# Kernel optimization log

Hardware: AMD Instinct MI355X
Metric: run time of the kernel (lower is better)

The kernel has to match this reference:

```python
import jax, jax.numpy as jnp
import numpy as np

E = 8          # num_experts
K = 2          # experts_per_token
D = 1024       # d_model
F = 2048       # dim_feedforward
B, S = 2, 2048

def setup_inputs() -> dict:
    key = jax.random.key(0)
    ks = jax.random.split(key, 5)
    scale = 0.02
    return {
        "x":   jax.random.normal(ks[0], (B, S, D), jnp.float32),
        "Wr":  jax.random.normal(ks[1], (E, D), jnp.float32) * scale,
        "temp": jnp.ones((1,), jnp.float32),
        "W1":  jax.random.normal(ks[2], (E, 2 * F, D), jnp.float32) * scale,
        "b1":  jnp.zeros((E, 2 * F), jnp.float32),
        "W2":  jax.random.normal(ks[3], (E, D, F), jnp.float32) * scale,
        "b2":  jnp.zeros((E, D), jnp.float32),
    }

def reference(x, Wr, temp, W1, b1, W2, b2):
    b, s, d = x.shape
    xf = x.reshape(-1, d)                                   # [T, D]
    router_logits = (xf @ Wr.T) / temp                      # [T, E]
    # eval mode: no router noise, dropout is identity
    top_w, top_idx = jax.lax.top_k(router_logits, K)        # [T, K]
    top_w = jax.nn.softmax(top_w, axis=-1)                  # renormalize over top-k
    # dense gate matrix [T, E]: weight if expert selected else 0 (topk indices are distinct)
    gates = jnp.sum(jax.nn.one_hot(top_idx, E, dtype=xf.dtype) * top_w[..., None], axis=1)
    out = jnp.zeros_like(xf)
    for e in range(E):  # fixed small expert loop, dense compute gated to zero for unrouted tokens
        h = xf @ W1[e].T + b1[e]                            # [T, 2F]
        a = h[:, :F] * jax.nn.silu(h[:, F:])                # SwiGLU -> [T, F]
        y = a @ W2[e].T + b2[e]                             # [T, D]
        out = out + y * gates[:, e:e + 1]
    return out.reshape(b, s, d)
```

## Files before the change

kernel.cpp:

```cpp
#include <hip/hip_runtime.h>
#include <hip/hip_bf16.h>

#define DEV __device__ __forceinline__

namespace {

constexpr int D     = 1024;
constexpr int F     = 2048;
constexpr int E     = 8;
constexpr int TWO_F = 2 * F;

typedef short bf16x8 __attribute__((ext_vector_type(8)));
typedef float f32x4  __attribute__((ext_vector_type(4)));

DEV unsigned short f32_to_bf16(float f) {
  unsigned int u = __builtin_bit_cast(unsigned int, f);
  u += 0x7fffu + ((u >> 16) & 1u);
  return (unsigned short)(u >> 16);
}

DEV void load_lds16(const void* g, void* l) {
  __builtin_amdgcn_global_load_lds((const __attribute__((address_space(1))) void*)g,
                                   (__attribute__((address_space(3))) void*)l, 16, 0, 0);
}

DEV const bf16x8* frag_addr(const unsigned short* S, int row, int kk, int quad) {
  int cl = (((kk >> 3) + quad) ^ (row & 7));
  return (const bf16x8*)(S + row * 64 + cl * 8);
}

__global__ void zero_kernel(float* __restrict__ p, int n4) {
  int i = blockIdx.x * 256 + threadIdx.x;
  if (i < n4) ((float4*)p)[i] = make_float4(0.f, 0.f, 0.f, 0.f);
}

__global__ void cvt_all_kernel(const float* __restrict__ x, const float* __restrict__ W1,
                               const float* __restrict__ W2,
                               unsigned short* __restrict__ xb, unsigned short* __restrict__ W1b,
                               unsigned short* __restrict__ W2b,
                               long long nx, long long n1) {
  long long i = (long long)(blockIdx.x * 256 + threadIdx.x) * 8;
  const float* src;
  unsigned short* dst;
  long long off;
  if (i < nx)            { src = x;  dst = xb;  off = i; }
  else if (i < nx + n1)  { src = W1; dst = W1b; off = i - nx; }
  else                   { src = W2; dst = W2b; off = i - nx - n1; }
  float4 a = *(const float4*)(src + off);
  float4 b = *(const float4*)(src + off + 4);
  uint4 o;
  o.x = (unsigned)f32_to_bf16(a.x) | ((unsigned)f32_to_bf16(a.y) << 16);
  o.y = (unsigned)f32_to_bf16(a.z) | ((unsigned)f32_to_bf16(a.w) << 16);
  o.z = (unsigned)f32_to_bf16(b.x) | ((unsigned)f32_to_bf16(b.y) << 16);
  o.w = (unsigned)f32_to_bf16(b.z) | ((unsigned)f32_to_bf16(b.w) << 16);
  *(uint4*)(dst + off) = o;
}

__global__ void router_kernel(const float* __restrict__ x, const float* __restrict__ Wr,
                              const float* __restrict__ temp,
                              int* __restrict__ topk_idx, float* __restrict__ topk_gate, int T) {
  int wid  = blockIdx.x * 4 + (threadIdx.x >> 6);
  int lane = threadIdx.x & 63;
  if (wid >= T) return;
  const float* xr = x + (size_t)wid * D;
  float acc[E];
#pragma unroll
  for (int e = 0; e < E; ++e) acc[e] = 0.f;
  int base = lane * 16;
#pragma unroll
  for (int u = 0; u < 4; ++u) {
    float4 xv = *(const float4*)(xr + base + u * 4);
#pragma unroll
    for (int e = 0; e < E; ++e) {
      float4 wv = *(const float4*)(Wr + e * D + base + u * 4);
      acc[e] += xv.x * wv.x + xv.y * wv.y + xv.z * wv.z + xv.w * wv.w;
    }
  }
#pragma unroll
  for (int e = 0; e < E; ++e) {
    float v = acc[e];
#pragma unroll
    for (int off = 32; off > 0; off >>= 1) v += __shfl_xor(v, off, 64);
    acc[e] = v;
  }
  if (lane == 0) {
    float inv = 1.0f / temp[0];
    float l[E];
#pragma unroll
    for (int e = 0; e < E; ++e) l[e] = acc[e] * inv;
    int e0 = 0;
#pragma unroll
    for (int e = 1; e < E; ++e) if (l[e] > l[e0]) e0 = e;
    int e1 = (e0 == 0) ? 1 : 0;
#pragma unroll
    for (int e = 0; e < E; ++e) if (e != e0 && l[e] > l[e1]) e1 = e;
    float dlt = l[e1] - l[e0];
    float ed  = __expf(dlt);
    topk_idx[2 * wid]      = e0;
    topk_idx[2 * wid + 1]  = e1;
    topk_gate[2 * wid]     = 1.f / (1.f + ed);
    topk_gate[2 * wid + 1] = ed / (1.f + ed);
  }
}

__global__ __launch_bounds__(1024)
void assign_kernel(const int* __restrict__ topk_idx, const float* __restrict__ topk_gate,
                   int* __restrict__ counts, int* __restrict__ offsets,
                   int* __restrict__ row_token, float* __restrict__ row_gate, int T) {
  __shared__ int hist[E];
  __shared__ int cur[E];
  const int tid = threadIdx.x;
  if (tid < E) hist[tid] = 0;
  __syncthreads();
  for (int t = tid; t < T; t += 1024) {
    atomicAdd(&hist[topk_idx[2 * t]], 1);
    atomicAdd(&hist[topk_idx[2 * t + 1]], 1);
  }
  __syncthreads();
  if (tid == 0) {
    int s = 0;
    for (int e = 0; e < E; ++e) {
      int c = hist[e];
      counts[e]  = c;
      offsets[e] = s;
      cur[e]     = s;
      s += c;
    }
  }
  __syncthreads();
  for (int t = tid; t < T; t += 1024) {
#pragma unroll
    for (int s = 0; s < 2; ++s) {
      int e = topk_idx[2 * t + s];
      int p = atomicAdd(&cur[e], 1);
      row_token[p] = t;
      row_gate[p]  = topk_gate[2 * t + s];
    }
  }
}

__global__ __launch_bounds__(256, 2)
void gemm1_kernel(const unsigned short* __restrict__ xb,
                  const unsigned short* __restrict__ W1b,
                  const float* __restrict__ b1,
                  const int* __restrict__ counts, const int* __restrict__ offsets,
                  const int* __restrict__ row_token,
                  unsigned short* __restrict__ a_buf) {
  const int e  = blockIdx.z;
  const int m0 = blockIdx.y * 128;
  const int n0 = blockIdx.x * 64;
  const int cnt = counts[e];
  if (m0 >= cnt) return;
  const int pairBase = offsets[e];

  __shared__ __align__(16) unsigned short As[128 * 64];
  __shared__ __align__(16) unsigned short Bs[128 * 64];
  __shared__ int tokS[128];

  const int tid = threadIdx.x;
  if (tid < 128) {
    int r = m0 + tid;
    tokS[tid] = (r < cnt) ? row_token[pairBase + r] : row_token[pairBase];
  }
  __syncthreads();

  const int lane = tid & 63;
  const int wave = tid >> 6;
  const int quad = lane >> 4;
  const int l16  = lane & 15;
  const int lr   = lane >> 3;
  const int lc   = lane & 7;
  const int sw   = lc ^ (lr & 7);
  const int wr   = wave >> 1;
  const int wc   = wave & 1;

  const unsigned short* W1e = W1b + (size_t)e * TWO_F * D;
  const unsigned short* aptr[4];
  const unsigned short* bptr[4];
#pragma unroll
  for (int i = 0; i < 4; ++i) {
    int r = wave * 32 + i * 8 + lr;
    aptr[i] = xb + (size_t)tokS[r] * D + sw * 8;
    int g = r >> 5, s = r & 31;
    int wrow = (g & 1) * F + n0 + (g >> 1) * 32 + s;
    bptr[i] = W1e + (size_t)wrow * D + sw * 8;
  }
  unsigned short* AsW = As + (wave * 32) * 64;
  unsigned short* BsW = Bs + (wave * 32) * 64;

  f32x4 acc[4][4];
#pragma unroll
  for (int i = 0; i < 4; ++i)
#pragma unroll
    for (int j = 0; j < 4; ++j) acc[i][j] = (f32x4){0.f, 0.f, 0.f, 0.f};

  for (int k0 = 0; k0 < D; k0 += 64) {
#pragma unroll
    for (int i = 0; i < 4; ++i) load_lds16(aptr[i] + k0, AsW + i * 8 * 64);
#pragma unroll
    for (int i = 0; i < 4; ++i) load_lds16(bptr[i] + k0, BsW + i * 8 * 64);
    __syncthreads();
#pragma unroll
    for (int kk = 0; kk < 64; kk += 32) {
      bf16x8 af[4], bf[4];
#pragma unroll
      for (int i = 0; i < 4; ++i)
        af[i] = *frag_addr(As, wr * 64 + i * 16 + l16, kk, quad);
#pragma unroll
      for (int j = 0; j < 4; ++j)
        bf[j] = *frag_addr(Bs, wc * 64 + j * 16 + l16, kk, quad);
#pragma unroll
      for (int i = 0; i < 4; ++i)
#pragma unroll
        for (int j = 0; j < 4; ++j)
          acc[i][j] = __builtin_amdgcn_mfma_f32_16x16x32_bf16(af[i], bf[j], acc[i][j], 0, 0, 0);
    }
    __syncthreads();
  }

#pragma unroll
  for (int i = 0; i < 4; ++i) {
    int rb = wr * 64 + i * 16 + quad * 4;
#pragma unroll
    for (int j = 0; j < 2; ++j) {
      int col = n0 + wc * 32 + j * 16 + l16;
      float bh1 = b1[e * TWO_F + col];
      float bh2 = b1[e * TWO_F + F + col];
#pragma unroll
      for (int rg = 0; rg < 4; ++rg) {
        int r = rb + rg;
        if (m0 + r < cnt) {
          float h1 = acc[i][j][rg] + bh1;
          float h2 = acc[i][j + 2][rg] + bh2;
          float a  = h1 * (h2 / (1.f + __expf(-h2)));
          a_buf[(size_t)(pairBase + m0 + r) * F + col] = f32_to_bf16(a);
        }
      }
    }
  }
}

__global__ __launch_bounds__(256, 2)
void gemm2_kernel(const unsigned short* __restrict__ a_buf,
                  const unsigned short* __restrict__ W2b,
                  const float* __restrict__ b2,
                  const int* __restrict__ counts, const int* __restrict__ offsets,
                  const int* __restrict__ row_token, const float* __restrict__ row_gate,
                  float* __restrict__ out, int totalPairs) {
  const int e  = blockIdx.z;
  const int m0 = blockIdx.y * 128;
  const int n0 = blockIdx.x * 128;
  const int cnt = counts[e];
  if (m0 >= cnt) return;
  const int pairBase = offsets[e];

  __shared__ __align__(16) unsigned short As[128 * 64];
  __shared__ __align__(16) unsigned short Bs[128 * 64];
  __shared__ int   tokS[128];
  __shared__ float gateS[128];

  const int tid = threadIdx.x;
  if (tid < 128) {
    int r = m0 + tid;
    bool v = (r < cnt);
    tokS[tid]  = v ? row_token[pairBase + r] : 0;
    gateS[tid] = v ? row_gate[pairBase + r] : 0.f;
  }
  __syncthreads();

  const int lane = tid & 63;
  const int wave = tid >> 6;
  const int quad = lane >> 4;
  const int l16  = lane & 15;
  const int lr   = lane >> 3;
  const int lc   = lane & 7;
  const int sw   = lc ^ (lr & 7);
  const int wr   = wave >> 1;
  const int wc   = wave & 1;

  const unsigned short* W2e = W2b + (size_t)e * D * F;
  const unsigned short* aptr[4];
  const unsigned short* bptr[4];
#pragma unroll
  for (int i = 0; i < 4; ++i) {
    int r = wave * 32 + i * 8 + lr;
    int g = pairBase + m0 + r;
    if (g > totalPairs - 1) g = totalPairs - 1;
    aptr[i] = a_buf + (size_t)g * F + sw * 8;
    bptr[i] = W2e + (size_t)(n0 + r) * F + sw * 8;
  }
  unsigned short* AsW = As + (wave * 32) * 64;
  unsigned short* BsW = Bs + (wave * 32) * 64;

  f32x4 acc[4][4];
#pragma unroll
  for (int i = 0; i < 4; ++i)
#pragma unroll
    for (int j = 0; j < 4; ++j) acc[i][j] = (f32x4){0.f, 0.f, 0.f, 0.f};

  for (int k0 = 0; k0 < F; k0 += 64) {
#pragma unroll
    for (int i = 0; i < 4; ++i) load_lds16(aptr[i] + k0, AsW + i * 8 * 64);
#pragma unroll
    for (int i = 0; i < 4; ++i) load_lds16(bptr[i] + k0, BsW + i * 8 * 64);
    __syncthreads();
#pragma unroll
    for (int kk = 0; kk < 64; kk += 32) {
      bf16x8 af[4], bf[4];
#pragma unroll
      for (int i = 0; i < 4; ++i)
        af[i] = *frag_addr(As, wr * 64 + i * 16 + l16, kk, quad);
#pragma unroll
      for (int j = 0; j < 4; ++j)
        bf[j] = *frag_addr(Bs, wc * 64 + j * 16 + l16, kk, quad);
#pragma unroll
      for (int i = 0; i < 4; ++i)
#pragma unroll
        for (int j = 0; j < 4; ++j)
          acc[i][j] = __builtin_amdgcn_mfma_f32_16x16x32_bf16(af[i], bf[j], acc[i][j], 0, 0, 0);
    }
    __syncthreads();
  }

#pragma unroll
  for (int j = 0; j < 4; ++j) {
    int col = n0 + wc * 64 + j * 16 + l16;
    float b2v = b2[e * D + col];
#pragma unroll
    for (int i = 0; i < 4; ++i) {
      int rb = wr * 64 + i * 16 + quad * 4;
#pragma unroll
      for (int rg = 0; rg < 4; ++rg) {
        int r = rb + rg;
        if (m0 + r < cnt) {
          float y = (acc[i][j][rg] + b2v) * gateS[r];
          atomicAdd(&out[(size_t)tokS[r] * D + col], y);
        }
      }
    }
  }
}

}

extern "C" void kernel_launch(void* const* d_in, const int* in_sizes, int n_in,
                              void* d_out, int out_size, void* d_ws, size_t ws_size,
                              hipStream_t stream) {
  (void)n_in; (void)out_size; (void)ws_size;
  const float* x    = (const float*)d_in[0];
  const float* Wr   = (const float*)d_in[1];
  const float* temp = (const float*)d_in[2];
  const float* W1   = (const float*)d_in[3];
  const float* b1   = (const float*)d_in[4];
  const float* W2   = (const float*)d_in[5];
  const float* b2   = (const float*)d_in[6];
  float* out = (float*)d_out;
  const int T = in_sizes[0] / D;

  char* ws = (char*)d_ws;
  size_t off = 0;
  unsigned short* xb    = (unsigned short*)(ws + off); off += (size_t)T * D * 2;
  unsigned short* W1b   = (unsigned short*)(ws + off); off += (size_t)E * TWO_F * D * 2;
  unsigned short* W2b   = (unsigned short*)(ws + off); off += (size_t)E * D * F * 2;
  unsigned short* a_buf = (unsigned short*)(ws + off); off += (size_t)T * 2 * F * 2;
  int*   counts    = (int*)(ws + off); off += 64;
  int*   offsets   = (int*)(ws + off); off += 64;
  int*   topk_idx  = (int*)(ws + off); off += (size_t)T * 2 * 4;
  float* topk_gate = (float*)(ws + off); off += (size_t)T * 2 * 4;
  int*   row_token = (int*)(ws + off); off += (size_t)T * 2 * 4;
  float* row_gate  = (float*)(ws + off); off += (size_t)T * 2 * 4;

  const long long nx = (long long)T * D;
  const long long n1 = (long long)E * TWO_F * D;
  const long long n2 = (long long)E * D * F;

  zero_kernel<<<(T * D / 4 + 255) / 256, 256, 0, stream>>>(out, T * D / 4);
  router_kernel<<<(T + 3) / 4, 256, 0, stream>>>(x, Wr, temp, topk_idx, topk_gate, T);
  assign_kernel<<<1, 1024, 0, stream>>>(topk_idx, topk_gate, counts, offsets,
                                        row_token, row_gate, T);
  cvt_all_kernel<<<(int)((nx + n1 + n2) / 2048), 256, 0, stream>>>(x, W1, W2, xb, W1b, W2b,
                                                                   nx, n1);
  gemm1_kernel<<<dim3(F / 64, (T * 2 + 127) / 128, E), 256, 0, stream>>>(xb, W1b, b1, counts,
                                                                         offsets, row_token, a_buf);
  gemm2_kernel<<<dim3(D / 128, (T * 2 + 127) / 128, E), 256, 0, stream>>>(a_buf, W2b, b2, counts,
                                                                          offsets, row_token,
                                                                          row_gate, out, T * 2);
}
```

Measured before the change: 477.2 us.

## Widen GEMM tiles to 512 threads with triple-buffered async LDS pipeline

Both expert GEMMs move from 256 to 512 threads per block and double the N tile, to 128x256 in the B dimension. Global-to-LDS loads become triple-buffered, prefetching two k-tiles ahead with explicit vmcnt waits and raw s_barrier instead of a full syncthreads per step. MFMA priority is raised around the compute. The aim is to overlap memory latency with matrix math and reuse each A tile across more columns. The cost is about 144KB of LDS per block, which probably limits occupancy to one block per CU, plus hand-tuned waitcnt values that must match the exact load count.

```diff
diff --git a/kernel.cpp b/kernel.cpp
--- a/kernel.cpp
+++ b/kernel.cpp
@@ -139,7 +139,8 @@
   }
 }
 
-__global__ __launch_bounds__(256, 2)
+
+__global__ __launch_bounds__(512, 2)
 void gemm1_kernel(const unsigned short* __restrict__ xb,
                   const unsigned short* __restrict__ W1b,
                   const float* __restrict__ b1,
@@ -148,13 +149,13 @@
                   unsigned short* __restrict__ a_buf) {
   const int e  = blockIdx.z;
   const int m0 = blockIdx.y * 128;
-  const int n0 = blockIdx.x * 64;
+  const int bx = blockIdx.x;
   const int cnt = counts[e];
   if (m0 >= cnt) return;
   const int pairBase = offsets[e];
 
-  __shared__ __align__(16) unsigned short As[128 * 64];
-  __shared__ __align__(16) unsigned short Bs[128 * 64];
+  __shared__ __align__(16) unsigned short As[3][128 * 64];
+  __shared__ __align__(16) unsigned short Bs[3][256 * 64];
   __shared__ int tokS[128];
 
   const int tid = threadIdx.x;
@@ -170,23 +171,33 @@
   const int l16  = lane & 15;
   const int lr   = lane >> 3;
   const int lc   = lane & 7;
-  const int sw   = lc ^ (lr & 7);
-  const int wr   = wave >> 1;
-  const int wc   = wave & 1;
+  const int sw   = lc ^ lr;
+  const int wr   = wave >> 2;
+  const int wc   = wave & 3;
 
   const unsigned short* W1e = W1b + (size_t)e * TWO_F * D;
-  const unsigned short* aptr[4];
-  const unsigned short* bptr[4];
+  const unsigned short* aSrc[2];
+  const unsigned short* bSrc[4];
+#pragma unroll
+  for (int i = 0; i < 2; ++i) {
+    int rA = i * 64 + wave * 8 + lr;
+    aSrc[i] = xb + (size_t)tokS[rA] * D + sw * 8;
+  }
 #pragma unroll
   for (int i = 0; i < 4; ++i) {
-    int r = wave * 32 + i * 8 + lr;
-    aptr[i] = xb + (size_t)tokS[r] * D + sw * 8;
-    int g = r >> 5, s = r & 31;
-    int wrow = (g & 1) * F + n0 + (g >> 1) * 32 + s;
-    bptr[i] = W1e + (size_t)wrow * D + sw * 8;
-  }
-  unsigned short* AsW = As + (wave * 32) * 64;
-  unsigned short* BsW = Bs + (wave * 32) * 64;
+    int rB = i * 64 + wave * 8 + lr;
+    int wrow = ((rB >> 5) & 1) * F + bx * 128 + (rB >> 6) * 32 + (rB & 31);
+    bSrc[i] = W1e + (size_t)wrow * D + sw * 8;
+  }
+
+  auto stage = [&](int t, int b) {
+#pragma unroll
+    for (int i = 0; i < 2; ++i)
+      load_lds16(aSrc[i] + t * 64, &As[b][(i * 64 + wave * 8) * 64]);
+#pragma unroll
+    for (int i = 0; i < 4; ++i)
+      load_lds16(bSrc[i] + t * 64, &Bs[b][(i * 64 + wave * 8) * 64]);
+  };
 
   f32x4 acc[4][4];
 #pragma unroll
@@ -194,28 +205,49 @@
 #pragma unroll
     for (int j = 0; j < 4; ++j) acc[i][j] = (f32x4){0.f, 0.f, 0.f, 0.f};
 
-  for (int k0 = 0; k0 < D; k0 += 64) {
-#pragma unroll
-    for (int i = 0; i < 4; ++i) load_lds16(aptr[i] + k0, AsW + i * 8 * 64);
-#pragma unroll
-    for (int i = 0; i < 4; ++i) load_lds16(bptr[i] + k0, BsW + i * 8 * 64);
-    __syncthreads();
-#pragma unroll
-    for (int kk = 0; kk < 64; kk += 32) {
-      bf16x8 af[4], bf[4];
-#pragma unroll
-      for (int i = 0; i < 4; ++i)
-        af[i] = *frag_addr(As, wr * 64 + i * 16 + l16, kk, quad);
+  constexpr int NT = D / 64;
+  stage(0, 0);
+  stage(1, 1);
+  int buf = 0;
+  for (int t = 0; t < NT; ++t) {
+    if (t + 2 < NT) {
+      int nb = buf + 2; if (nb >= 3) nb -= 3;
+      stage(t + 2, nb);
+      asm volatile("s_waitcnt vmcnt(12)" ::: "memory");
+    } else if (t + 1 < NT) {
+      asm volatile("s_waitcnt vmcnt(6)" ::: "memory");
+    } else {
+      asm volatile("s_waitcnt vmcnt(0)" ::: "memory");
+    }
+    __builtin_amdgcn_sched_barrier(0);
+    __builtin_amdgcn_s_barrier();
+    __builtin_amdgcn_sched_barrier(0);
+    const unsigned short* Ab = As[buf];
+    const unsigned short* Bb = Bs[buf];
+    bf16x8 a0[4], b0[4], a1[4], b1f[4];
+#pragma unroll
+    for (int i = 0; i < 4; ++i) a0[i]  = *frag_addr(Ab, wr * 64 + i * 16 + l16, 0,  quad);
+#pragma unroll
+    for (int j = 0; j < 4; ++j) b0[j]  = *frag_addr(Bb, wc * 64 + j * 16 + l16, 0,  quad);
+#pragma unroll
+    for (int i = 0; i < 4; ++i) a1[i]  = *frag_addr(Ab, wr * 64 + i * 16 + l16, 32, quad);
+#pragma unroll
+    for (int j = 0; j < 4; ++j) b1f[j] = *frag_addr(Bb, wc * 64 + j * 16 + l16, 32, quad);
+    __builtin_amdgcn_s_setprio(1);
+#pragma unroll
+    for (int i = 0; i < 4; ++i)
 #pragma unroll
       for (int j = 0; j < 4; ++j)
-        bf[j] = *frag_addr(Bs, wc * 64 + j * 16 + l16, kk, quad);
-#pragma unroll
-      for (int i = 0; i < 4; ++i)
-#pragma unroll
-        for (int j = 0; j < 4; ++j)
-          acc[i][j] = __builtin_amdgcn_mfma_f32_16x16x32_bf16(af[i], bf[j], acc[i][j], 0, 0, 0);
-    }
-    __syncthreads();
+        acc[i][j] = __builtin_amdgcn_mfma_f32_16x16x32_bf16(a0[i], b0[j], acc[i][j], 0, 0, 0);
+#pragma unroll
+    for (int i = 0; i < 4; ++i)
+#pragma unroll
+      for (int j = 0; j < 4; ++j)
+        acc[i][j] = __builtin_amdgcn_mfma_f32_16x16x32_bf16(a1[i], b1f[j], acc[i][j], 0, 0, 0);
+    __builtin_amdgcn_s_setprio(0);
+    __builtin_amdgcn_sched_barrier(0);
+    __builtin_amdgcn_s_barrier();
+    ++buf; if (buf >= 3) buf = 0;
   }
 
 #pragma unroll
@@ -223,7 +255,7 @@
     int rb = wr * 64 + i * 16 + quad * 4;
 #pragma unroll
     for (int j = 0; j < 2; ++j) {
-      int col = n0 + wc * 32 + j * 16 + l16;
+      int col = bx * 128 + wc * 32 + j * 16 + l16;
       float bh1 = b1[e * TWO_F + col];
       float bh2 = b1[e * TWO_F + F + col];
 #pragma unroll
@@ -240,7 +272,7 @@
   }
 }
 
-__global__ __launch_bounds__(256, 2)
+__global__ __launch_bounds__(512, 2)
 void gemm2_kernel(const unsigned short* __restrict__ a_buf,
                   const unsigned short* __restrict__ W2b,
                   const float* __restrict__ b2,
@@ -249,13 +281,13 @@
                   float* __restrict__ out, int totalPairs) {
   const int e  = blockIdx.z;
   const int m0 = blockIdx.y * 128;
-  const int n0 = blockIdx.x * 128;
+  const int bx = blockIdx.x;
   const int cnt = counts[e];
   if (m0 >= cnt) return;
   const int pairBase = offsets[e];
 
-  __shared__ __align__(16) unsigned short As[128 * 64];
-  __shared__ __align__(16) unsigned short Bs[128 * 64];
+  __shared__ __align__(16) unsigned short As[3][128 * 64];
+  __shared__ __align__(16) unsigned short Bs[3][256 * 64];
   __shared__ int   tokS[128];
   __shared__ float gateS[128];
 
@@ -274,23 +306,34 @@
   const int l16  = lane & 15;
   const int lr   = lane >> 3;
   const int lc   = lane & 7;
-  const int sw   = lc ^ (lr & 7);
-  const int wr   = wave >> 1;
-  const int wc   = wave & 1;
+  const int sw   = lc ^ lr;
+  const int wr   = wave >> 2;
+  const int wc   = wave & 3;
 
   const unsigned short* W2e = W2b + (size_t)e * D * F;
-  const unsigned short* aptr[4];
-  const unsigned short* bptr[4];
+  const unsigned short* aSrc[2];
+  const unsigned short* bSrc[4];
+#pragma unroll
+  for (int i = 0; i < 2; ++i) {
+    int rA = i * 64 + wave * 8 + lr;
+    int g = pairBase + m0 + rA;
+    if (g > totalPairs - 1) g = totalPairs - 1;
+    aSrc[i] = a_buf + (size_t)g * F + sw * 8;
+  }
 #pragma unroll
   for (int i = 0; i < 4; ++i) {
-    int r = wave * 32 + i * 8 + lr;
-    int g = pairBase + m0 + r;
-    if (g > totalPairs - 1) g = totalPairs - 1;
-    aptr[i] = a_buf + (size_t)g * F + sw * 8;
-    bptr[i] = W2e + (size_t)(n0 + r) * F + sw * 8;
-  }
-  unsigned short* AsW = As + (wave * 32) * 64;
-  unsigned short* BsW = Bs + (wave * 32) * 64;
+    int rB = i * 64 + wave * 8 + lr;
+    bSrc[i] = W2e + (size_t)(bx * 256 + rB) * F + sw * 8;
+  }
+
+  auto stage = [&](int t, int b) {
+#pragma unroll
+    for (int i = 0; i < 2; ++i)
+      load_lds16(aSrc[i] + t * 64, &As[b][(i * 64 + wave * 8) * 64]);
+#pragma unroll
+    for (int i = 0; i < 4; ++i)
+      load_lds16(bSrc[i] + t * 64, &Bs[b][(i * 64 + wave * 8) * 64]);
+  };
 
   f32x4 acc[4][4];
 #pragma unroll
@@ -298,33 +341,54 @@
 #pragma unroll
     for (int j = 0; j < 4; ++j) acc[i][j] = (f32x4){0.f, 0.f, 0.f, 0.f};
 
-  for (int k0 = 0; k0 < F; k0 += 64) {
-#pragma unroll
-    for (int i = 0; i < 4; ++i) load_lds16(aptr[i] + k0, AsW + i * 8 * 64);
-#pragma unroll
-    for (int i = 0; i < 4; ++i) load_lds16(bptr[i] + k0, BsW + i * 8 * 64);
-    __syncthreads();
-#pragma unroll
-    for (int kk = 0; kk < 64; kk += 32) {
-      bf16x8 af[4], bf[4];
-#pragma unroll
-      for (int i = 0; i < 4; ++i)
-        af[i] = *frag_addr(As, wr * 64 + i * 16 + l16, kk, quad);
+  constexpr int NT = F / 64;
+  stage(0, 0);
+  stage(1, 1);
+  int buf = 0;
+  for (int t = 0; t < NT; ++t) {
+    if (t + 2 < NT) {
+      int nb = buf + 2; if (nb >= 3) nb -= 3;
+      stage(t + 2, nb);
+      asm volatile("s_waitcnt vmcnt(12)" ::: "memory");
+    } else if (t + 1 < NT) {
+      asm volatile("s_waitcnt vmcnt(6)" ::: "memory");
+    } else {
+      asm volatile("s_waitcnt vmcnt(0)" ::: "memory");
+    }
+    __builtin_amdgcn_sched_barrier(0);
+    __builtin_amdgcn_s_barrier();
+    __builtin_amdgcn_sched_barrier(0);
+    const unsigned short* Ab = As[buf];
+    const unsigned short* Bb = Bs[buf];
+    bf16x8 a0[4], b0[4], a1[4], b1f[4];
+#pragma unroll
+    for (int i = 0; i < 4; ++i) a0[i]  = *frag_addr(Ab, wr * 64 + i * 16 + l16, 0,  quad);
+#pragma unroll
+    for (int j = 0; j < 4; ++j) b0[j]  = *frag_addr(Bb, wc * 64 + j * 16 + l16, 0,  quad);
+#pragma unroll
+    for (int i = 0; i < 4; ++i) a1[i]  = *frag_addr(Ab, wr * 64 + i * 16 + l16, 32, quad);
+#pragma unroll
+    for (int j = 0; j < 4; ++j) b1f[j] = *frag_addr(Bb, wc * 64 + j * 16 + l16, 32, quad);
+    __builtin_amdgcn_s_setprio(1);
+#pragma unroll
+    for (int i = 0; i < 4; ++i)
 #pragma unroll
       for (int j = 0; j < 4; ++j)
-        bf[j] = *frag_addr(Bs, wc * 64 + j * 16 + l16, kk, quad);
-#pragma unroll
-      for (int i = 0; i < 4; ++i)
-#pragma unroll
-        for (int j = 0; j < 4; ++j)
-          acc[i][j] = __builtin_amdgcn_mfma_f32_16x16x32_bf16(af[i], bf[j], acc[i][j], 0, 0, 0);
-    }
-    __syncthreads();
+        acc[i][j] = __builtin_amdgcn_mfma_f32_16x16x32_bf16(a0[i], b0[j], acc[i][j], 0, 0, 0);
+#pragma unroll
+    for (int i = 0; i < 4; ++i)
+#pragma unroll
+      for (int j = 0; j < 4; ++j)
+        acc[i][j] = __builtin_amdgcn_mfma_f32_16x16x32_bf16(a1[i], b1f[j], acc[i][j], 0, 0, 0);
+    __builtin_amdgcn_s_setprio(0);
+    __builtin_amdgcn_sched_barrier(0);
+    __builtin_amdgcn_s_barrier();
+    ++buf; if (buf >= 3) buf = 0;
   }
 
 #pragma unroll
   for (int j = 0; j < 4; ++j) {
-    int col = n0 + wc * 64 + j * 16 + l16;
+    int col = bx * 256 + wc * 64 + j * 16 + l16;
     float b2v = b2[e * D + col];
 #pragma unroll
     for (int i = 0; i < 4; ++i) {
@@ -380,9 +444,9 @@
                                         row_token, row_gate, T);
   cvt_all_kernel<<<(int)((nx + n1 + n2) / 2048), 256, 0, stream>>>(x, W1, W2, xb, W1b, W2b,
                                                                    nx, n1);
-  gemm1_kernel<<<dim3(F / 64, (T * 2 + 127) / 128, E), 256, 0, stream>>>(xb, W1b, b1, counts,
-                                                                         offsets, row_token, a_buf);
-  gemm2_kernel<<<dim3(D / 128, (T * 2 + 127) / 128, E), 256, 0, stream>>>(a_buf, W2b, b2, counts,
-                                                                          offsets, row_token,
-                                                                          row_gate, out, T * 2);
-}
+  gemm1_kernel<<<dim3(F / 128, 32, E), 512, 0, stream>>>(xb, W1b, b1, counts,
+                                                         offsets, row_token, a_buf);
+  gemm2_kernel<<<dim3(D / 256, 32, E), 512, 0, stream>>>(a_buf, W2b, b2, counts,
+                                                         offsets, row_token,
+                                                         row_gate, out, T * 2);
+}
```

New measurement: 567.0 us. 1.19x slower.

## Double-buffer LDS tiles in both expert GEMMs to overlap loads with MFMA

Applied to the files above, without the earlier changes.

Both grouped GEMM kernels now use two LDS buffers and prefetch the next K tile via direct global-to-LDS loads while computing the current one. Manual vmcnt waits and raw s_barriers replace the two __syncthreads per iteration. The grid's M dimension shrinks to 32 tiles per expert, which removes blocks that would exit immediately. LDS usage per block doubles, which can limit occupancy.

```diff
diff --git a/kernel.cpp b/kernel.cpp
--- a/kernel.cpp
+++ b/kernel.cpp
@@ -139,6 +139,7 @@
   }
 }
 
+
 __global__ __launch_bounds__(256, 2)
 void gemm1_kernel(const unsigned short* __restrict__ xb,
                   const unsigned short* __restrict__ W1b,
@@ -153,8 +154,8 @@
   if (m0 >= cnt) return;
   const int pairBase = offsets[e];
 
-  __shared__ __align__(16) unsigned short As[128 * 64];
-  __shared__ __align__(16) unsigned short Bs[128 * 64];
+  __shared__ __align__(16) unsigned short As[2][128 * 64];
+  __shared__ __align__(16) unsigned short Bs[2][128 * 64];
   __shared__ int tokS[128];
 
   const int tid = threadIdx.x;
@@ -170,7 +171,7 @@
   const int l16  = lane & 15;
   const int lr   = lane >> 3;
   const int lc   = lane & 7;
-  const int sw   = lc ^ (lr & 7);
+  const int sw   = lc ^ lr;
   const int wr   = wave >> 1;
   const int wc   = wave & 1;
 
@@ -185,8 +186,15 @@
     int wrow = (g & 1) * F + n0 + (g >> 1) * 32 + s;
     bptr[i] = W1e + (size_t)wrow * D + sw * 8;
   }
-  unsigned short* AsW = As + (wave * 32) * 64;
-  unsigned short* BsW = Bs + (wave * 32) * 64;
+
+  auto stage = [&](int t, int b) {
+#pragma unroll
+    for (int i = 0; i < 4; ++i)
+      load_lds16(aptr[i] + t * 64, &As[b][(wave * 32 + i * 8) * 64]);
+#pragma unroll
+    for (int i = 0; i < 4; ++i)
+      load_lds16(bptr[i] + t * 64, &Bs[b][(wave * 32 + i * 8) * 64]);
+  };
 
   f32x4 acc[4][4];
 #pragma unroll
@@ -194,28 +202,39 @@
 #pragma unroll
     for (int j = 0; j < 4; ++j) acc[i][j] = (f32x4){0.f, 0.f, 0.f, 0.f};
 
-  for (int k0 = 0; k0 < D; k0 += 64) {
-#pragma unroll
-    for (int i = 0; i < 4; ++i) load_lds16(aptr[i] + k0, AsW + i * 8 * 64);
-#pragma unroll
-    for (int i = 0; i < 4; ++i) load_lds16(bptr[i] + k0, BsW + i * 8 * 64);
-    __syncthreads();
+  constexpr int NT = D / 64;
+  stage(0, 0);
+  int buf = 0;
+  for (int t = 0; t < NT; ++t) {
+    if (t + 1 < NT) {
+      stage(t + 1, buf ^ 1);
+      asm volatile("s_waitcnt vmcnt(8)" ::: "memory");
+    } else {
+      asm volatile("s_waitcnt vmcnt(0)" ::: "memory");
+    }
+    __builtin_amdgcn_sched_barrier(0);
+    __builtin_amdgcn_s_barrier();
+    __builtin_amdgcn_sched_barrier(0);
+    const unsigned short* Ab = As[buf];
+    const unsigned short* Bb = Bs[buf];
 #pragma unroll
     for (int kk = 0; kk < 64; kk += 32) {
       bf16x8 af[4], bf[4];
 #pragma unroll
       for (int i = 0; i < 4; ++i)
-        af[i] = *frag_addr(As, wr * 64 + i * 16 + l16, kk, quad);
+        af[i] = *frag_addr(Ab, wr * 64 + i * 16 + l16, kk, quad);
 #pragma unroll
       for (int j = 0; j < 4; ++j)
-        bf[j] = *frag_addr(Bs, wc * 64 + j * 16 + l16, kk, quad);
+        bf[j] = *frag_addr(Bb, wc * 64 + j * 16 + l16, kk, quad);
 #pragma unroll
       for (int i = 0; i < 4; ++i)
 #pragma unroll
         for (int j = 0; j < 4; ++j)
           acc[i][j] = __builtin_amdgcn_mfma_f32_16x16x32_bf16(af[i], bf[j], acc[i][j], 0, 0, 0);
     }
-    __syncthreads();
+    __builtin_amdgcn_sched_barrier(0);
+    __builtin_amdgcn_s_barrier();
+    buf ^= 1;
   }
 
 #pragma unroll
@@ -254,8 +273,8 @@
   if (m0 >= cnt) return;
   const int pairBase = offsets[e];
 
-  __shared__ __align__(16) unsigned short As[128 * 64];
-  __shared__ __align__(16) unsigned short Bs[128 * 64];
+  __shared__ __align__(16) unsigned short As[2][128 * 64];
+  __shared__ __align__(16) unsigned short Bs[2][128 * 64];
   __shared__ int   tokS[128];
   __shared__ float gateS[128];
 
@@ -274,7 +293,7 @@
   const int l16  = lane & 15;
   const int lr   = lane >> 3;
   const int lc   = lane & 7;
-  const int sw   = lc ^ (lr & 7);
+  const int sw   = lc ^ lr;
   const int wr   = wave >> 1;
   const int wc   = wave & 1;
 
@@ -289,8 +308,15 @@
     aptr[i] = a_buf + (size_t)g * F + sw * 8;
     bptr[i] = W2e + (size_t)(n0 + r) * F + sw * 8;
   }
-  unsigned short* AsW = As + (wave * 32) * 64;
-  unsigned short* BsW = Bs + (wave * 32) * 64;
+
+  auto stage = [&](int t, int b) {
+#pragma unroll
+    for (int i = 0; i < 4; ++i)
+      load_lds16(aptr[i] + t * 64, &As[b][(wave * 32 + i * 8) * 64]);
+#pragma unroll
+    for (int i = 0; i < 4; ++i)
+      load_lds16(bptr[i] + t * 64, &Bs[b][(wave * 32 + i * 8) * 64]);
+  };
 
   f32x4 acc[4][4];
 #pragma unroll
@@ -298,28 +324,39 @@
 #pragma unroll
     for (int j = 0; j < 4; ++j) acc[i][j] = (f32x4){0.f, 0.f, 0.f, 0.f};
 
-  for (int k0 = 0; k0 < F; k0 += 64) {
-#pragma unroll
-    for (int i = 0; i < 4; ++i) load_lds16(aptr[i] + k0, AsW + i * 8 * 64);
-#pragma unroll
-    for (int i = 0; i < 4; ++i) load_lds16(bptr[i] + k0, BsW + i * 8 * 64);
-    __syncthreads();
+  constexpr int NT = F / 64;
+  stage(0, 0);
+  int buf = 0;
+  for (int t = 0; t < NT; ++t) {
+    if (t + 1 < NT) {
+      stage(t + 1, buf ^ 1);
+      asm volatile("s_waitcnt vmcnt(8)" ::: "memory");
+    } else {
+      asm volatile("s_waitcnt vmcnt(0)" ::: "memory");
+    }
+    __builtin_amdgcn_sched_barrier(0);
+    __builtin_amdgcn_s_barrier();
+    __builtin_amdgcn_sched_barrier(0);
+    const unsigned short* Ab = As[buf];
+    const unsigned short* Bb = Bs[buf];
 #pragma unroll
     for (int kk = 0; kk < 64; kk += 32) {
       bf16x8 af[4], bf[4];
 #pragma unroll
       for (int i = 0; i < 4; ++i)
-        af[i] = *frag_addr(As, wr * 64 + i * 16 + l16, kk, quad);
+        af[i] = *frag_addr(Ab, wr * 64 + i * 16 + l16, kk, quad);
 #pragma unroll
       for (int j = 0; j < 4; ++j)
-        bf[j] = *frag_addr(Bs, wc * 64 + j * 16 + l16, kk, quad);
+        bf[j] = *frag_addr(Bb, wc * 64 + j * 16 + l16, kk, quad);
 #pragma unroll
       for (int i = 0; i < 4; ++i)
 #pragma unroll
         for (int j = 0; j < 4; ++j)
           acc[i][j] = __builtin_amdgcn_mfma_f32_16x16x32_bf16(af[i], bf[j], acc[i][j], 0, 0, 0);
     }
-    __syncthreads();
+    __builtin_amdgcn_sched_barrier(0);
+    __builtin_amdgcn_s_barrier();
+    buf ^= 1;
   }
 
 #pragma unroll
@@ -380,9 +417,9 @@
                                         row_token, row_gate, T);
   cvt_all_kernel<<<(int)((nx + n1 + n2) / 2048), 256, 0, stream>>>(x, W1, W2, xb, W1b, W2b,
                                                                    nx, n1);
-  gemm1_kernel<<<dim3(F / 64, (T * 2 + 127) / 128, E), 256, 0, stream>>>(xb, W1b, b1, counts,
-                                                                         offsets, row_token, a_buf);
-  gemm2_kernel<<<dim3(D / 128, (T * 2 + 127) / 128, E), 256, 0, stream>>>(a_buf, W2b, b2, counts,
-                                                                          offsets, row_token,
-                                                                          row_gate, out, T * 2);
-}
+  gemm1_kernel<<<dim3(F / 64, 32, E), 256, 0, stream>>>(xb, W1b, b1, counts,
+                                                        offsets, row_token, a_buf);
+  gemm2_kernel<<<dim3(D / 128, 32, E), 256, 0, stream>>>(a_buf, W2b, b2, counts,
+                                                         offsets, row_token,
+                                                         row_gate, out, T * 2);
+}
```

Result: slower. 530.7 us (+11.2%).
